# Kernel optimization log

Hardware: AMD Instinct MI355X
Metric: run time of the kernel (lower is better)

## Reference

```python
import jax, jax.numpy as jnp
import numpy as np

NUM_ITER = 4
MIN_DISP = 1.0 / 100.0  # 1/max_depth
MAX_DISP = 1.0 / 0.1    # 1/min_depth


def _diag_embed(v):
    return v[..., :, None] * jnp.eye(v.shape[-1], dtype=v.dtype)


def _v2m(r):  # r: [B,3,1] -> antisymmetric [B,3,3]
    a1, a2, a3 = r[:, 0, 0], r[:, 1, 0], r[:, 2, 0]
    z = jnp.zeros_like(a1)
    return jnp.stack([z, -a3, a2, a3, z, -a1, -a2, a1, z], axis=-1).reshape(-1, 3, 3)


def _se3_pose(se3):  # se3: [B,6,1] -> [B,3,4]
    B = se3.shape[0]
    t, w = se3[:, 0:3], se3[:, 3:6]
    Nr = jnp.maximum(jnp.sqrt(jnp.sum(w * w, axis=1, keepdims=True)), 1e-12)  # [B,1,1]
    r = w / Nr
    I = jnp.eye(3, dtype=se3.dtype)[None]
    rx = _v2m(r)
    c, s = jnp.cos(Nr), jnp.sin(Nr)
    R = c * I + (1.0 - c) * jnp.matmul(r, jnp.transpose(r, (0, 2, 1))) + s * rx
    J = I + (Nr - s) / Nr * jnp.matmul(rx, rx) + (1.0 - c) / Nr * rx
    T = jnp.matmul(J, t)
    return jnp.concatenate([R, T], axis=2)


def _homogeneous(p34):
    B = p34.shape[0]
    ext = jnp.broadcast_to(jnp.array([[[0.0, 0.0, 0.0, 1.0]]], dtype=p34.dtype), (B, 1, 4))
    return jnp.concatenate([p34, ext], axis=1)


def _project_2d3d(points, depth, K_inv):  # [B,2,N],[B,1,N] -> [B,3,N]
    ones = jnp.ones_like(points[:, :1])
    xy3d = jnp.concatenate([points, ones], axis=1)
    return jnp.matmul(K_inv, xy3d) * depth


def _project_3d2d(p3d, K):
    q = jnp.matmul(K, p3d)
    return q[:, 0:2] / jnp.maximum(q[:, 2:3], 0.01)


def _reproject_error(p1, p2, disp, pose, K, K_inv):
    depth = 1.0 / jnp.maximum(disp, 0.01)
    p3d = _project_2d3d(p1, depth, K_inv)
    p3d_hat = jnp.matmul(pose[:, :3, :3], p3d) + pose[:, :3, 3:]
    return p2 - _project_3d2d(p3d_hat, K)


def _mean_on_mask(data, mask):  # reduce over last (point) dim, keepdims
    return jnp.sum(data * mask, axis=2, keepdims=True) / jnp.sum(mask, axis=2, keepdims=True)


def _jacobi_pose(p3d, K):  # -> [B,2,6,N]
    B, _, N = p3d.shape
    fx, fy = K[:, 0:1, 0:1], K[:, 1:2, 1:2]
    X, Y = p3d[:, 0:1], p3d[:, 1:2]
    Z = jnp.maximum(p3d[:, 2:3], 1e-12)
    iZ = 1.0 / Z
    iZ2 = iZ * iZ
    z = jnp.zeros_like(X)
    rows = [fx * iZ, z, -fx * X * iZ2, -fx * X * Y * iZ2, fx + fx * X * X * iZ2, -fx * Y * iZ,
            z, fy * iZ, -fy * Y * iZ2, -fy - fy * Y * Y * iZ2, fy * X * Y * iZ2, fy * X * iZ]
    return -jnp.concatenate(rows, axis=1).reshape(B, 2, 6, N)


def _jacobi_disp(p3d, pose, disps):  # -> [B,2,1,N]
    B, _, N = p3d.shape
    fx, fy = K0 = pose  # placeholder avoided below
    raise NotImplementedError


def _jacobi_disp_impl(p3d, pose, K, disps):  # -> [B,2,1,N]
    B, _, N = p3d.shape
    fx, fy = K[:, 0:1, 0:1], K[:, 1:2, 1:2]
    X, Y = p3d[:, 0:1], p3d[:, 1:2]
    Z = jnp.maximum(p3d[:, 2:3], 1e-12)
    iZ = 1.0 / Z
    iZ2 = iZ * iZ
    z = jnp.zeros_like(X)
    J1 = jnp.concatenate([fx * iZ, z, -fx * X * iZ2, z, fy * iZ, -fy * Y * iZ2], axis=1)
    J1 = jnp.transpose(J1.reshape(B, 2, 3, N), (0, 3, 1, 2))  # [B,N,2,3]
    T = pose[:, :3, 3:]  # [B,3,1]
    DD = -1.0 / disps    # [B,1,N]
    J2 = jnp.concatenate([DD * (X - T[:, 0:1]), (Y - T[:, 1:2]) * DD, (Z - T[:, 2:3]) * DD], axis=1)
    J2 = jnp.transpose(J2.reshape(B, 3, 1, N), (0, 3, 1, 2))  # [B,N,3,1]
    J = -jnp.matmul(J1, J2)                                   # [B,N,2,1]
    return jnp.transpose(J, (0, 2, 3, 1))                     # [B,2,1,N]


def _huber_w(err, mask, b=9.0):  # diag values of the [B,N,2,2] weight -> [B,N,2]
    B, _, N = err.shape
    en = jnp.sqrt(jnp.sum(err * err, axis=1, keepdims=True))          # [B,1,N]
    w = jnp.minimum(b / jnp.maximum(en, 1e-12), 1.0)
    w = jnp.sqrt(w) * mask                                            # [B,1,N]
    w = jnp.broadcast_to(jnp.transpose(w, (0, 2, 1)), (B, N, 2))
    return jax.lax.stop_gradient(w)


def _marginalization(Bm, E, C, V, W, L):
    Bsz, N = E.shape[0], E.shape[1]
    Bm = Bm + _diag_embed(jnp.diagonal(Bm, axis1=-2, axis2=-1)) * L   # L:[B,1,1]
    C = C + C * L.reshape(Bsz, 1, 1, 1)                               # C diag is itself (1x1)
    C_inv = 1.0 / jnp.maximum(C, 1.0)
    Bm = Bm + jnp.eye(6, dtype=Bm.dtype)
    Ev = E[..., 0]                 # [B,N,6]
    cinv = C_inv[:, :, 0, 0]       # [B,N]
    Wv = W[:, :, 0, 0]             # [B,N]
    Hsc = jnp.einsum('bn,bni,bnj->bij', cinv, Ev, Ev) / N
    bsc = (jnp.einsum('bn,bni,bn->bi', cinv, Ev, Wv) / N)[..., None]  # [B,6,1]
    invL = 1.0 / (1.0 + L)
    left = Bm - Hsc * invL
    right = V - bsc * invL
    s = 1.0 / jnp.sqrt(jnp.diagonal(left, axis1=-2, axis2=-1) + 10.0)  # [B,6]
    D = _diag_embed(s)
    H = D @ left @ D
    delta_pose = D @ jnp.linalg.solve(H, D @ right)                   # [B,6,1]
    p3d_sc = jnp.einsum('bni,bi->bn', Ev, delta_pose[:, :, 0]) * invL[:, 0, 0][:, None]
    delta_points = cinv * (Wv - p3d_sc)                               # [B,N]
    return delta_pose, delta_points


def _lm_step(pts_coord, pts_disp, pose, K, K_inv, mask, L):
    B, _, N = pts_coord.shape
    pts_depth = 1.0 / pts_disp
    p3d = _project_2d3d(pts_coord[:, 0:2], pts_depth, K_inv)
    p3d_hat = jnp.matmul(pose[:, :3, :3], p3d) + pose[:, :3, 3:]
    p2d_hat = _project_3d2d(p3d_hat, K)
    errors = pts_coord[:, 2:4] - p2d_hat                     # [B,2,N]
    J_pose = _jacobi_pose(p3d_hat, K)                        # [B,2,6,N]
    J_disp = _jacobi_disp_impl(p3d_hat, pose, K, pts_disp)   # [B,2,1,N]
    w = _huber_w(errors, mask)                               # [B,N,2]
    w2 = w * w
    Jp_T = jnp.transpose(J_pose, (0, 3, 2, 1))               # [B,N,6,2]
    Jd_T = jnp.transpose(J_disp, (0, 3, 2, 1))               # [B,N,1,2]
    Jp = jnp.transpose(J_pose, (0, 3, 1, 2))                 # [B,N,2,6]
    Jd = jnp.transpose(J_disp, (0, 3, 1, 2))                 # [B,N,2,1]
    Bm = jnp.einsum('bnik,bnkj->bij', Jp_T * w2[:, :, None, :], Jp) / N
    E = jnp.matmul(Jp_T * w2[:, :, None, :], Jd)             # [B,N,6,1]
    C = jnp.matmul(Jd_T * w2[:, :, None, :], Jd)             # [B,N,1,1]
    e = jnp.transpose(errors, (0, 2, 1))[..., None]          # [B,N,2,1]
    g_pose = -jnp.einsum('bnik,bnkj->bij', Jp_T * w[:, :, None, :], e) / N  # [B,6,1]
    g_disp = -jnp.matmul(Jd_T * w[:, :, None, :], e)         # [B,N,1,1]
    delta_pose, delta_points = _marginalization(Bm, E, C, g_pose, g_disp, L)
    return delta_pose, delta_points[:, None, :]              # [B,6,1], [B,1,N]


def reference(pts_coord, pts_disp, pose, K, K_inv, mask, L):
    for _ in range(NUM_ITER):
        dp, dd = _lm_step(pts_coord, pts_disp, pose, K, K_inv, mask, L)
        disp_new = jnp.clip(pts_disp + dd, MIN_DISP, MAX_DISP)
        pose_new = jnp.matmul(_homogeneous(_se3_pose(dp)), pose)
        e1 = _reproject_error(pts_coord[:, 0:2], pts_coord[:, 2:4], disp_new, pose_new, K, K_inv)
        e2 = _reproject_error(pts_coord[:, 0:2], pts_coord[:, 2:4], pts_disp, pose, K, K_inv)
        r1 = _mean_on_mask(jnp.linalg.norm(e1, axis=1, keepdims=True), mask)
        r2 = _mean_on_mask(jnp.linalg.norm(e2, axis=1, keepdims=True), mask)
        M = jax.lax.stop_gradient((r1 < r2).astype(pose.dtype))  # [B,1,1]
        pts_disp = jnp.where(M == 1, disp_new, pts_disp)
        pose = jnp.where(M == 1, pose_new, pose)
        L = jnp.clip(jnp.where(M == 1, L * 0.5, L * 5.0), 0.01, 1e6)
    return pose, pts_disp


def setup_inputs() -> dict:
    B, N = 8, 131072
    W, H = 640, 480
    key = jax.random.key(0)
    k = jax.random.split(key, 4)
    p1 = jax.random.uniform(k[0], (B, 2, N), dtype=jnp.float32) * jnp.array([W, H], jnp.float32).reshape(1, 2, 1)
    p2 = p1 + jax.random.normal(k[1], (B, 2, N), dtype=jnp.float32) * 2.0
    pts_coord = jnp.concatenate([p1, p2], axis=1)                      # [B,4,N]
    pts_disp = jax.random.uniform(k[2], (B, 1, N), dtype=jnp.float32, minval=0.05, maxval=2.0)
    pose = jnp.tile(jnp.eye(4, dtype=jnp.float32)[None], (B, 1, 1))
    pose = pose.at[:, :3, 3].set(jax.random.normal(k[3], (B, 3), dtype=jnp.float32) * 0.05)
    K = jnp.tile(jnp.array([[320.0, 0.0, 320.0], [0.0, 320.0, 240.0], [0.0, 0.0, 1.0]], jnp.float32)[None], (B, 1, 1))
    K_inv = jnp.linalg.inv(K)
    mask = jnp.ones((B, 1, N), jnp.float32)
    L = jnp.ones((B, 1, 1), jnp.float32) * 0.01
    return {'pts_coord': pts_coord, 'pts_disp': pts_disp, 'pose': pose, 'K': K, 'K_inv': K_inv, 'mask': mask, 'L': L}
```

## Files before the change

kernel.cpp:

```cpp
#include <hip/hip_runtime.h>
#include <math.h>


constexpr int TPB  = 256;
constexpr int BLKA = 64;
constexpr int NRED = 54;

__device__ __forceinline__ float wave_red(float v) {
#pragma unroll
  for (int m = 32; m; m >>= 1) v += __shfl_xor(v, m, 64);
  return v;
}

__device__ __forceinline__ float reproj_norm(
    float x1, float y1, float x2, float y2, float d,
    const float* P, const float* Kc, const float* Ki) {
  float depth = 1.0f / fmaxf(d, 0.01f);
  float pxx = (Ki[0]*x1 + Ki[1]*y1 + Ki[2]) * depth;
  float pyy = (Ki[3]*x1 + Ki[4]*y1 + Ki[5]) * depth;
  float pzz = (Ki[6]*x1 + Ki[7]*y1 + Ki[8]) * depth;
  float X = P[0]*pxx + P[1]*pyy + P[2]*pzz + P[3];
  float Y = P[4]*pxx + P[5]*pyy + P[6]*pzz + P[7];
  float Z = P[8]*pxx + P[9]*pyy + P[10]*pzz + P[11];
  float q0 = Kc[0]*X + Kc[1]*Y + Kc[2]*Z;
  float q1 = Kc[3]*X + Kc[4]*Y + Kc[5]*Z;
  float q2 = Kc[6]*X + Kc[7]*Y + Kc[8]*Z;
  float iZc = 1.0f / fmaxf(q2, 0.01f);
  float ex = x2 - q0*iZc, ey = y2 - q1*iZc;
  return sqrtf(ex*ex + ey*ey);
}

__global__ __launch_bounds__(TPB) void kpassA(
    const float* __restrict__ pts, const float* __restrict__ disp_src,
    const float* __restrict__ prop, const float* __restrict__ mask,
    const float* __restrict__ Kin, const float* __restrict__ Kiin,
    float* __restrict__ disp_cur, const float* __restrict__ pose_cur,
    const float* __restrict__ Lc, const float* __restrict__ flags,
    float* __restrict__ partA, int N) {
  const int b = blockIdx.y;
  float Kc[9], Ki[9], P[12];
#pragma unroll
  for (int i = 0; i < 9; i++) { Kc[i] = Kin[b*9+i]; Ki[i] = Kiin[b*9+i]; }
#pragma unroll
  for (int i = 0; i < 12; i++) P[i] = pose_cur[b*16+i];
  const float Lval = Lc[b];
  const float onepL = 1.0f + Lval;
  const float fsel = flags[b];
  const float fx = Kc[0], fy = Kc[4];

  float acc[NRED];
#pragma unroll
  for (int k = 0; k < NRED; k++) acc[k] = 0.0f;

  const size_t bN = (size_t)b * N;
  const float* px1 = pts + (size_t)b*4*N;
  const float* py1 = px1 + N;
  const float* px2 = px1 + 2*(size_t)N;
  const float* py2 = px1 + 3*(size_t)N;

  for (int n = blockIdx.x*TPB + threadIdx.x; n < N; n += gridDim.x*TPB) {
    float x1 = px1[n], y1 = py1[n], x2 = px2[n], y2 = py2[n];
    float d = disp_src[bN+n];
    if (fsel != 0.0f) d = prop[bN+n];
    disp_cur[bN+n] = d;
    float m = mask[bN+n];

    float depth = 1.0f / d;
    float pxx = (Ki[0]*x1 + Ki[1]*y1 + Ki[2]) * depth;
    float pyy = (Ki[3]*x1 + Ki[4]*y1 + Ki[5]) * depth;
    float pzz = (Ki[6]*x1 + Ki[7]*y1 + Ki[8]) * depth;
    float X = P[0]*pxx + P[1]*pyy + P[2]*pzz + P[3];
    float Y = P[4]*pxx + P[5]*pyy + P[6]*pzz + P[7];
    float Z = P[8]*pxx + P[9]*pyy + P[10]*pzz + P[11];
    float q0 = Kc[0]*X + Kc[1]*Y + Kc[2]*Z;
    float q1 = Kc[3]*X + Kc[4]*Y + Kc[5]*Z;
    float q2 = Kc[6]*X + Kc[7]*Y + Kc[8]*Z;
    float iZc = 1.0f / fmaxf(q2, 0.01f);
    float ex = x2 - q0*iZc;
    float ey = y2 - q1*iZc;
    float iZ = 1.0f / fmaxf(Z, 1e-12f);
    float iZ2 = iZ*iZ;

    float jp0[6], jp1[6];
    jp0[0] = -(fx*iZ);  jp0[1] = 0.0f;       jp0[2] = fx*X*iZ2;
    jp0[3] = fx*X*Y*iZ2; jp0[4] = -(fx + fx*X*X*iZ2); jp0[5] = fx*Y*iZ;
    jp1[0] = 0.0f;      jp1[1] = -(fy*iZ);   jp1[2] = fy*Y*iZ2;
    jp1[3] = fy + fy*Y*Y*iZ2; jp1[4] = -(fy*X*Y*iZ2); jp1[5] = -(fy*X*iZ);

    float DD = -depth;
    float dx = X - P[3], dy = Y - P[7], dz = Z - P[11];
    float jd0 = -((fx*iZ)*(DD*dx) - (fx*X*iZ2)*(DD*dz));
    float jd1 = -((fy*iZ)*(DD*dy) - (fy*Y*iZ2)*(DD*dz));

    float en = sqrtf(ex*ex + ey*ey);
    float wmin = fminf(9.0f / fmaxf(en, 1e-12f), 1.0f);
    float w  = sqrtf(wmin) * m;
    float w2 = w * w;

    float E[6];
#pragma unroll
    for (int k = 0; k < 6; k++) E[k] = w2*(jp0[k]*jd0 + jp1[k]*jd1);
    float C = w2*(jd0*jd0 + jd1*jd1);
    float cinv = 1.0f / fmaxf(C*onepL, 1.0f);
    float Wv = -w*(jd0*ex + jd1*ey);

    int idx = 0;
#pragma unroll
    for (int k = 0; k < 6; k++)
#pragma unroll
      for (int l = k; l < 6; l++) { acc[idx] += w2*(jp0[k]*jp0[l] + jp1[k]*jp1[l]); idx++; }
#pragma unroll
    for (int k = 0; k < 6; k++) acc[21+k] -= w*(jp0[k]*ex + jp1[k]*ey);
    idx = 27;
#pragma unroll
    for (int k = 0; k < 6; k++)
#pragma unroll
      for (int l = k; l < 6; l++) { acc[idx] += (cinv*E[k])*E[l]; idx++; }
#pragma unroll
    for (int k = 0; k < 6; k++) acc[48+k] += cinv*E[k]*Wv;
  }

  __shared__ float lds[TPB/64][NRED];
  const int lane = threadIdx.x & 63, wvi = threadIdx.x >> 6;
#pragma unroll
  for (int k = 0; k < NRED; k++) {
    float v = wave_red(acc[k]);
    if (lane == 0) lds[wvi][k] = v;
  }
  __syncthreads();
  if (threadIdx.x < NRED) {
    float s = 0.0f;
#pragma unroll
    for (int wq = 0; wq < TPB/64; wq++) s += lds[wq][threadIdx.x];
    partA[((size_t)b*gridDim.x + blockIdx.x)*NRED + threadIdx.x] = s;
  }
}

__global__ __launch_bounds__(64) void ksolve(
    const float* __restrict__ partA, int nblk,
    const float* __restrict__ Lc, const float* __restrict__ pose_cur,
    float* __restrict__ pose_new, float* __restrict__ dpose, int N) {
  const int b = blockIdx.x;
  __shared__ float S[NRED];
  const int t = threadIdx.x;
  if (t < NRED) {
    float s = 0.0f;
    for (int j = 0; j < nblk; j++) s += partA[((size_t)b*nblk + j)*NRED + t];
    S[t] = s;
  }
  __syncthreads();
  if (t != 0) return;

  const float invN = 1.0f / (float)N;
  float Bm[6][6], Hs[6][6], g[6], bs[6];
  {
    int idx = 0;
    for (int k = 0; k < 6; k++)
      for (int l = k; l < 6; l++) { float v = S[idx++]*invN; Bm[k][l] = v; Bm[l][k] = v; }
    for (int k = 0; k < 6; k++) g[k] = S[21+k]*invN;
    idx = 27;
    for (int k = 0; k < 6; k++)
      for (int l = k; l < 6; l++) { float v = S[idx++]*invN; Hs[k][l] = v; Hs[l][k] = v; }
    for (int k = 0; k < 6; k++) bs[k] = S[48+k]*invN;
  }
  const float L = Lc[b];
  const float invL = 1.0f / (1.0f + L);
  float left[6][6], right[6];
  for (int k = 0; k < 6; k++) {
    for (int l = 0; l < 6; l++) {
      float v = Bm[k][l] - Hs[k][l]*invL;
      if (k == l) v += Bm[k][k]*L + 1.0f;
      left[k][l] = v;
    }
    right[k] = g[k] - bs[k]*invL;
  }
  float sv[6];
  for (int k = 0; k < 6; k++) sv[k] = 1.0f / sqrtf(left[k][k] + 10.0f);
  float H[6][7];
  for (int k = 0; k < 6; k++) {
    for (int l = 0; l < 6; l++) H[k][l] = sv[k]*left[k][l]*sv[l];
    H[k][6] = sv[k]*right[k];
  }
  for (int c = 0; c < 6; c++) {
    int piv = c; float mx = fabsf(H[c][c]);
    for (int r = c+1; r < 6; r++) { float a = fabsf(H[r][c]); if (a > mx) { mx = a; piv = r; } }
    if (piv != c)
      for (int cc2 = c; cc2 < 7; cc2++) { float tmp = H[c][cc2]; H[c][cc2] = H[piv][cc2]; H[piv][cc2] = tmp; }
    float ip = 1.0f / H[c][c];
    for (int r = c+1; r < 6; r++) {
      float f = H[r][c]*ip;
      for (int cc2 = c; cc2 < 7; cc2++) H[r][cc2] -= f*H[c][cc2];
    }
  }
  float x[6];
  for (int c = 5; c >= 0; c--) {
    float v = H[c][6];
    for (int cc2 = c+1; cc2 < 6; cc2++) v -= H[c][cc2]*x[cc2];
    x[c] = v / H[c][c];
  }
  float dp[6];
  for (int k = 0; k < 6; k++) { dp[k] = sv[k]*x[k]; dpose[b*6+k] = dp[k]; }

  float tx = dp[0], ty = dp[1], tz = dp[2];
  float wx = dp[3], wy = dp[4], wz = dp[5];
  float Nr = fmaxf(sqrtf(wx*wx + wy*wy + wz*wz), 1e-12f);
  float rx = wx/Nr, ry = wy/Nr, rz = wz/Nr;
  float c_ = cosf(Nr), sn = sinf(Nr);
  float omc = 1.0f - c_;
  float SK[3][3] = {{0.0f,-rz,ry},{rz,0.0f,-rx},{-ry,rx,0.0f}};
  float SK2[3][3];
  for (int i = 0; i < 3; i++)
    for (int j = 0; j < 3; j++) {
      float s2 = 0.0f;
      for (int k = 0; k < 3; k++) s2 += SK[i][k]*SK[k][j];
      SK2[i][j] = s2;
    }
  float rr[3] = {rx, ry, rz};
  float a = (Nr - sn)/Nr, bcoef = omc/Nr;
  float R3[3][3], Jm[3][3];
  for (int i = 0; i < 3; i++)
    for (int j = 0; j < 3; j++) {
      float eye = (i == j) ? 1.0f : 0.0f;
      R3[i][j] = c_*eye + omc*rr[i]*rr[j] + sn*SK[i][j];
      Jm[i][j] = eye + a*SK2[i][j] + bcoef*SK[i][j];
    }
  float T3[3];
  for (int i = 0; i < 3; i++) T3[i] = Jm[i][0]*tx + Jm[i][1]*ty + Jm[i][2]*tz;
  float Pc[16];
  for (int i = 0; i < 16; i++) Pc[i] = pose_cur[b*16+i];
  float Pn[16];
  for (int i = 0; i < 3; i++)
    for (int j = 0; j < 4; j++)
      Pn[i*4+j] = R3[i][0]*Pc[j] + R3[i][1]*Pc[4+j] + R3[i][2]*Pc[8+j] + T3[i]*Pc[12+j];
  for (int j = 0; j < 4; j++) Pn[12+j] = Pc[12+j];
  for (int i = 0; i < 16; i++) pose_new[b*16+i] = Pn[i];
}

__global__ __launch_bounds__(TPB) void kpassB(
    const float* __restrict__ pts, const float* __restrict__ disp_cur,
    const float* __restrict__ mask,
    const float* __restrict__ Kin, const float* __restrict__ Kiin,
    const float* __restrict__ pose_cur, const float* __restrict__ pose_new,
    const float* __restrict__ Lc, const float* __restrict__ dpose,
    float* __restrict__ prop, float* __restrict__ partB, int N) {
  const int b = blockIdx.y;
  float Kc[9], Ki[9], P[12], Pn[12], dp[6];
#pragma unroll
  for (int i = 0; i < 9; i++) { Kc[i] = Kin[b*9+i]; Ki[i] = Kiin[b*9+i]; }
#pragma unroll
  for (int i = 0; i < 12; i++) { P[i] = pose_cur[b*16+i]; Pn[i] = pose_new[b*16+i]; }
#pragma unroll
  for (int i = 0; i < 6; i++) dp[i] = dpose[b*6+i];
  const float Lval = Lc[b];
  const float onepL = 1.0f + Lval;
  const float invL = 1.0f / onepL;
  const float fx = Kc[0], fy = Kc[4];

  float r1a = 0.0f, r2a = 0.0f, msa = 0.0f;
  const size_t bN = (size_t)b * N;
  const float* px1 = pts + (size_t)b*4*N;
  const float* py1 = px1 + N;
  const float* px2 = px1 + 2*(size_t)N;
  const float* py2 = px1 + 3*(size_t)N;

  for (int n = blockIdx.x*TPB + threadIdx.x; n < N; n += gridDim.x*TPB) {
    float x1 = px1[n], y1 = py1[n], x2 = px2[n], y2 = py2[n];
    float d = disp_cur[bN+n];
    float m = mask[bN+n];

    float depth = 1.0f / d;
    float pxx = (Ki[0]*x1 + Ki[1]*y1 + Ki[2]) * depth;
    float pyy = (Ki[3]*x1 + Ki[4]*y1 + Ki[5]) * depth;
    float pzz = (Ki[6]*x1 + Ki[7]*y1 + Ki[8]) * depth;
    float X = P[0]*pxx + P[1]*pyy + P[2]*pzz + P[3];
    float Y = P[4]*pxx + P[5]*pyy + P[6]*pzz + P[7];
    float Z = P[8]*pxx + P[9]*pyy + P[10]*pzz + P[11];
    float q0 = Kc[0]*X + Kc[1]*Y + Kc[2]*Z;
    float q1 = Kc[3]*X + Kc[4]*Y + Kc[5]*Z;
    float q2 = Kc[6]*X + Kc[7]*Y + Kc[8]*Z;
    float iZc = 1.0f / fmaxf(q2, 0.01f);
    float ex = x2 - q0*iZc;
    float ey = y2 - q1*iZc;
    float iZ = 1.0f / fmaxf(Z, 1e-12f);
    float iZ2 = iZ*iZ;

    float jp0[6], jp1[6];
    jp0[0] = -(fx*iZ);  jp0[1] = 0.0f;       jp0[2] = fx*X*iZ2;
    jp0[3] = fx*X*Y*iZ2; jp0[4] = -(fx + fx*X*X*iZ2); jp0[5] = fx*Y*iZ;
    jp1[0] = 0.0f;      jp1[1] = -(fy*iZ);   jp1[2] = fy*Y*iZ2;
    jp1[3] = fy + fy*Y*Y*iZ2; jp1[4] = -(fy*X*Y*iZ2); jp1[5] = -(fy*X*iZ);

    float DD = -depth;
    float dx = X - P[3], dy = Y - P[7], dz = Z - P[11];
    float jd0 = -((fx*iZ)*(DD*dx) - (fx*X*iZ2)*(DD*dz));
    float jd1 = -((fy*iZ)*(DD*dy) - (fy*Y*iZ2)*(DD*dz));

    float en = sqrtf(ex*ex + ey*ey);
    float wmin = fminf(9.0f / fmaxf(en, 1e-12f), 1.0f);
    float w  = sqrtf(wmin) * m;
    float w2 = w * w;

    float dotE = 0.0f;
#pragma unroll
    for (int k = 0; k < 6; k++) {
      float Ek = w2*(jp0[k]*jd0 + jp1[k]*jd1);
      dotE += Ek * dp[k];
    }
    float C = w2*(jd0*jd0 + jd1*jd1);
    float cinv = 1.0f / fmaxf(C*onepL, 1.0f);
    float Wv = -w*(jd0*ex + jd1*ey);

    float dnew = d + cinv*(Wv - dotE*invL);
    dnew = fminf(fmaxf(dnew, 0.01f), 10.0f);
    prop[bN+n] = dnew;

    float n1 = reproj_norm(x1, y1, x2, y2, dnew, Pn, Kc, Ki);
    float n2 = reproj_norm(x1, y1, x2, y2, d,    P,  Kc, Ki);
    r1a += n1*m; r2a += n2*m; msa += m;
  }

  __shared__ float lds[TPB/64][3];
  const int lane = threadIdx.x & 63, wvi = threadIdx.x >> 6;
  float v0 = wave_red(r1a), v1 = wave_red(r2a), v2 = wave_red(msa);
  if (lane == 0) { lds[wvi][0] = v0; lds[wvi][1] = v1; lds[wvi][2] = v2; }
  __syncthreads();
  if (threadIdx.x < 3) {
    float s = 0.0f;
#pragma unroll
    for (int wq = 0; wq < TPB/64; wq++) s += lds[wq][threadIdx.x];
    partB[((size_t)b*gridDim.x + blockIdx.x)*3 + threadIdx.x] = s;
  }
}

__global__ __launch_bounds__(256) void kupdate(
    int iter, const float* __restrict__ partB, int nblk,
    const float* __restrict__ pose_in, const float* __restrict__ L_in,
    float* __restrict__ pose_cur, const float* __restrict__ pose_new,
    float* __restrict__ Lc, float* __restrict__ flags, int B) {
  const int t = threadIdx.x;
  if (iter == 0) {
    if (t < B*16) pose_cur[t] = pose_in[t];
    if (t < B) { Lc[t] = L_in[t]; flags[t] = 0.0f; }
    return;
  }
  __shared__ float sM[16];
  if (t < B) {
    float r1 = 0.0f, r2 = 0.0f, ms = 0.0f;
    for (int j = 0; j < nblk; j++) {
      const float* p = partB + ((size_t)t*nblk + j)*3;
      r1 += p[0]; r2 += p[1]; ms += p[2];
    }
    float M = ((r1/ms) < (r2/ms)) ? 1.0f : 0.0f;
    sM[t] = M;
    flags[t] = M;
    float L = Lc[t];
    L = (M != 0.0f) ? L*0.5f : L*5.0f;
    Lc[t] = fminf(fmaxf(L, 0.01f), 1000000.0f);
  }
  __syncthreads();
  if (t < B*16) {
    int b = t >> 4;
    if (sM[b] != 0.0f) pose_cur[t] = pose_new[t];
  }
}

__global__ __launch_bounds__(TPB) void kout(
    const float* __restrict__ pose_cur, const float* __restrict__ flags,
    const float* __restrict__ prop, float* __restrict__ dout, int N, int B) {
  const int b = blockIdx.y;
  if (blockIdx.x == 0 && threadIdx.x < 16)
    dout[b*16 + threadIdx.x] = pose_cur[b*16 + threadIdx.x];
  if (flags[b] == 0.0f) return;
  float* dd = dout + B*16;
  const size_t bN = (size_t)b * N;
  for (int n = blockIdx.x*TPB + threadIdx.x; n < N; n += gridDim.x*TPB)
    dd[bN+n] = prop[bN+n];
}

extern "C" void kernel_launch(void* const* d_in, const int* in_sizes, int n_in,
                              void* d_out, int out_size, void* d_ws, size_t ws_size,
                              hipStream_t stream) {
  const float* pts   = (const float*)d_in[0];
  const float* disp0 = (const float*)d_in[1];
  const float* pose0 = (const float*)d_in[2];
  const float* Kin   = (const float*)d_in[3];
  const float* Kiin  = (const float*)d_in[4];
  const float* mask  = (const float*)d_in[5];
  const float* L0    = (const float*)d_in[6];

  const int B = in_sizes[6];
  const int N = in_sizes[1] / B;
  const size_t BN = (size_t)B * N;

  float* out      = (float*)d_out;
  float* disp_cur = out + B*16;

  float* ws       = (float*)d_ws;
  float* prop     = ws;
  float* partA    = prop + BN;
  float* partB    = partA + (size_t)B*BLKA*NRED;
  float* pose_cur = partB + (size_t)B*BLKA*3;
  float* pose_new = pose_cur + (size_t)B*16;
  float* Lc       = pose_new + (size_t)B*16;
  float* dpose    = Lc + B;
  float* flags    = dpose + (size_t)B*6;

  dim3 gridBig(BLKA, B), blk(TPB);
  for (int it = 0; it < 4; ++it) {
    kupdate<<<1, 256, 0, stream>>>(it, partB, BLKA, pose0, L0,
                                   pose_cur, pose_new, Lc, flags, B);
    kpassA<<<gridBig, blk, 0, stream>>>(pts, (it == 0) ? disp0 : disp_cur, prop,
                                        mask, Kin, Kiin, disp_cur, pose_cur,
                                        Lc, flags, partA, N);
    ksolve<<<dim3(B), dim3(64), 0, stream>>>(partA, BLKA, Lc, pose_cur,
                                             pose_new, dpose, N);
    kpassB<<<gridBig, blk, 0, stream>>>(pts, disp_cur, mask, Kin, Kiin,
                                        pose_cur, pose_new, Lc, dpose,
                                        prop, partB, N);
  }
  kupdate<<<1, 256, 0, stream>>>(4, partB, BLKA, pose0, L0,
                                 pose_cur, pose_new, Lc, flags, B);
  kout<<<gridBig, blk, 0, stream>>>(pose_cur, flags, prop, out, N, B);
}
```

Baseline: 349.5 us.

## Fold solve and update kernels into the streaming passes via redundant per-block compute

Drops the tiny kupdate and ksolve launches. Each block of the main passes now recomputes the accept decision, the damping update and the 6x6 LM solve redundantly, and block 0 persists the shared state. Pose and L are double-buffered across iterations so no block reads state that another block in the same kernel is writing. This cuts the launch count per iteration from 4 to 2, removing launch gaps, at the cost of serial single-thread solve work and extra partial-sum reads at the start of every block.

```diff
diff --git a/kernel.cpp b/kernel.cpp
--- a/kernel.cpp
+++ b/kernel.cpp
@@ -30,22 +30,61 @@
   return sqrtf(ex*ex + ey*ey);
 }
 
-__global__ __launch_bounds__(TPB) void kpassA(
+__device__ __forceinline__ float accept_M(const float* __restrict__ partB,
+                                          int b) {
+  float r1 = 0.0f, r2 = 0.0f, ms = 0.0f;
+  for (int j = 0; j < BLKA; j++) {
+    const float* p = partB + ((size_t)b*BLKA + j)*3;
+    r1 += p[0]; r2 += p[1]; ms += p[2];
+  }
+  return ((r1/ms) < (r2/ms)) ? 1.0f : 0.0f;
+}
+
+__global__ __launch_bounds__(TPB) void kA(
+    int it,
     const float* __restrict__ pts, const float* __restrict__ disp_src,
     const float* __restrict__ prop, const float* __restrict__ mask,
     const float* __restrict__ Kin, const float* __restrict__ Kiin,
-    float* __restrict__ disp_cur, const float* __restrict__ pose_cur,
-    const float* __restrict__ Lc, const float* __restrict__ flags,
+    float* __restrict__ disp_cur,
+    const float* __restrict__ pose0, const float* __restrict__ L0,
+    const float* __restrict__ partB, const float* __restrict__ pose_new_ws,
+    float* __restrict__ pose_slot_w, const float* __restrict__ pose_slot_r,
+    float* __restrict__ L_slot_w, const float* __restrict__ L_slot_r,
     float* __restrict__ partA, int N) {
   const int b = blockIdx.y;
+
+  __shared__ float sP[16];
+  __shared__ float sMeta[2];
+  if (threadIdx.x == 0) {
+    float P[16], Lv, fs;
+    if (it == 0) {
+      for (int i = 0; i < 16; i++) P[i] = pose0[b*16+i];
+      Lv = L0[b]; fs = 0.0f;
+    } else {
+      float M = accept_M(partB, b);
+      fs = M;
+      float Lp = L_slot_r[b];
+      float Ln = (M != 0.0f) ? Lp*0.5f : Lp*5.0f;
+      Lv = fminf(fmaxf(Ln, 0.01f), 1000000.0f);
+      for (int i = 0; i < 16; i++)
+        P[i] = (M != 0.0f) ? pose_new_ws[b*16+i] : pose_slot_r[b*16+i];
+    }
+    for (int i = 0; i < 16; i++) sP[i] = P[i];
+    sMeta[0] = fs; sMeta[1] = Lv;
+    if (blockIdx.x == 0) {
+      for (int i = 0; i < 16; i++) pose_slot_w[b*16+i] = P[i];
+      L_slot_w[b] = Lv;
+    }
+  }
+  __syncthreads();
+
   float Kc[9], Ki[9], P[12];
 #pragma unroll
   for (int i = 0; i < 9; i++) { Kc[i] = Kin[b*9+i]; Ki[i] = Kiin[b*9+i]; }
 #pragma unroll
-  for (int i = 0; i < 12; i++) P[i] = pose_cur[b*16+i];
-  const float Lval = Lc[b];
-  const float onepL = 1.0f + Lval;
-  const float fsel = flags[b];
+  for (int i = 0; i < 12; i++) P[i] = sP[i];
+  const float onepL = 1.0f + sMeta[1];
+  const float fsel = sMeta[0];
   const float fx = Kc[0], fy = Kc[4];
 
   float acc[NRED];
@@ -136,123 +175,123 @@
   }
 }
 
-__global__ __launch_bounds__(64) void ksolve(
-    const float* __restrict__ partA, int nblk,
-    const float* __restrict__ Lc, const float* __restrict__ pose_cur,
-    float* __restrict__ pose_new, float* __restrict__ dpose, int N) {
-  const int b = blockIdx.x;
-  __shared__ float S[NRED];
-  const int t = threadIdx.x;
-  if (t < NRED) {
-    float s = 0.0f;
-    for (int j = 0; j < nblk; j++) s += partA[((size_t)b*nblk + j)*NRED + t];
-    S[t] = s;
-  }
-  __syncthreads();
-  if (t != 0) return;
-
-  const float invN = 1.0f / (float)N;
-  float Bm[6][6], Hs[6][6], g[6], bs[6];
-  {
-    int idx = 0;
-    for (int k = 0; k < 6; k++)
-      for (int l = k; l < 6; l++) { float v = S[idx++]*invN; Bm[k][l] = v; Bm[l][k] = v; }
-    for (int k = 0; k < 6; k++) g[k] = S[21+k]*invN;
-    idx = 27;
-    for (int k = 0; k < 6; k++)
-      for (int l = k; l < 6; l++) { float v = S[idx++]*invN; Hs[k][l] = v; Hs[l][k] = v; }
-    for (int k = 0; k < 6; k++) bs[k] = S[48+k]*invN;
-  }
-  const float L = Lc[b];
-  const float invL = 1.0f / (1.0f + L);
-  float left[6][6], right[6];
-  for (int k = 0; k < 6; k++) {
-    for (int l = 0; l < 6; l++) {
-      float v = Bm[k][l] - Hs[k][l]*invL;
-      if (k == l) v += Bm[k][k]*L + 1.0f;
-      left[k][l] = v;
-    }
-    right[k] = g[k] - bs[k]*invL;
-  }
-  float sv[6];
-  for (int k = 0; k < 6; k++) sv[k] = 1.0f / sqrtf(left[k][k] + 10.0f);
-  float H[6][7];
-  for (int k = 0; k < 6; k++) {
-    for (int l = 0; l < 6; l++) H[k][l] = sv[k]*left[k][l]*sv[l];
-    H[k][6] = sv[k]*right[k];
-  }
-  for (int c = 0; c < 6; c++) {
-    int piv = c; float mx = fabsf(H[c][c]);
-    for (int r = c+1; r < 6; r++) { float a = fabsf(H[r][c]); if (a > mx) { mx = a; piv = r; } }
-    if (piv != c)
-      for (int cc2 = c; cc2 < 7; cc2++) { float tmp = H[c][cc2]; H[c][cc2] = H[piv][cc2]; H[piv][cc2] = tmp; }
-    float ip = 1.0f / H[c][c];
-    for (int r = c+1; r < 6; r++) {
-      float f = H[r][c]*ip;
-      for (int cc2 = c; cc2 < 7; cc2++) H[r][cc2] -= f*H[c][cc2];
-    }
-  }
-  float x[6];
-  for (int c = 5; c >= 0; c--) {
-    float v = H[c][6];
-    for (int cc2 = c+1; cc2 < 6; cc2++) v -= H[c][cc2]*x[cc2];
-    x[c] = v / H[c][c];
-  }
-  float dp[6];
-  for (int k = 0; k < 6; k++) { dp[k] = sv[k]*x[k]; dpose[b*6+k] = dp[k]; }
-
-  float tx = dp[0], ty = dp[1], tz = dp[2];
-  float wx = dp[3], wy = dp[4], wz = dp[5];
-  float Nr = fmaxf(sqrtf(wx*wx + wy*wy + wz*wz), 1e-12f);
-  float rx = wx/Nr, ry = wy/Nr, rz = wz/Nr;
-  float c_ = cosf(Nr), sn = sinf(Nr);
-  float omc = 1.0f - c_;
-  float SK[3][3] = {{0.0f,-rz,ry},{rz,0.0f,-rx},{-ry,rx,0.0f}};
-  float SK2[3][3];
-  for (int i = 0; i < 3; i++)
-    for (int j = 0; j < 3; j++) {
-      float s2 = 0.0f;
-      for (int k = 0; k < 3; k++) s2 += SK[i][k]*SK[k][j];
-      SK2[i][j] = s2;
-    }
-  float rr[3] = {rx, ry, rz};
-  float a = (Nr - sn)/Nr, bcoef = omc/Nr;
-  float R3[3][3], Jm[3][3];
-  for (int i = 0; i < 3; i++)
-    for (int j = 0; j < 3; j++) {
-      float eye = (i == j) ? 1.0f : 0.0f;
-      R3[i][j] = c_*eye + omc*rr[i]*rr[j] + sn*SK[i][j];
-      Jm[i][j] = eye + a*SK2[i][j] + bcoef*SK[i][j];
-    }
-  float T3[3];
-  for (int i = 0; i < 3; i++) T3[i] = Jm[i][0]*tx + Jm[i][1]*ty + Jm[i][2]*tz;
-  float Pc[16];
-  for (int i = 0; i < 16; i++) Pc[i] = pose_cur[b*16+i];
-  float Pn[16];
-  for (int i = 0; i < 3; i++)
-    for (int j = 0; j < 4; j++)
-      Pn[i*4+j] = R3[i][0]*Pc[j] + R3[i][1]*Pc[4+j] + R3[i][2]*Pc[8+j] + T3[i]*Pc[12+j];
-  for (int j = 0; j < 4; j++) Pn[12+j] = Pc[12+j];
-  for (int i = 0; i < 16; i++) pose_new[b*16+i] = Pn[i];
-}
-
-__global__ __launch_bounds__(TPB) void kpassB(
+__global__ __launch_bounds__(TPB) void kB(
     const float* __restrict__ pts, const float* __restrict__ disp_cur,
     const float* __restrict__ mask,
     const float* __restrict__ Kin, const float* __restrict__ Kiin,
-    const float* __restrict__ pose_cur, const float* __restrict__ pose_new,
-    const float* __restrict__ Lc, const float* __restrict__ dpose,
+    const float* __restrict__ pose_slot, const float* __restrict__ L_slot,
+    const float* __restrict__ partA,
+    float* __restrict__ pose_new_ws,
     float* __restrict__ prop, float* __restrict__ partB, int N) {
   const int b = blockIdx.y;
+  const float L = L_slot[b];
+
+  __shared__ float S[NRED];
+  __shared__ float sPn[16];
+  __shared__ float sdp[6];
+  if (threadIdx.x < NRED) {
+    float s = 0.0f;
+    for (int j = 0; j < BLKA; j++)
+      s += partA[((size_t)b*BLKA + j)*NRED + threadIdx.x];
+    S[threadIdx.x] = s;
+  }
+  __syncthreads();
+  if (threadIdx.x == 0) {
+    const float invN = 1.0f / (float)N;
+    float Bm[6][6], Hs[6][6], g[6], bs[6];
+    {
+      int idx = 0;
+      for (int k = 0; k < 6; k++)
+        for (int l = k; l < 6; l++) { float v = S[idx++]*invN; Bm[k][l] = v; Bm[l][k] = v; }
+      for (int k = 0; k < 6; k++) g[k] = S[21+k]*invN;
+      idx = 27;
+      for (int k = 0; k < 6; k++)
+        for (int l = k; l < 6; l++) { float v = S[idx++]*invN; Hs[k][l] = v; Hs[l][k] = v; }
+      for (int k = 0; k < 6; k++) bs[k] = S[48+k]*invN;
+    }
+    const float invL = 1.0f / (1.0f + L);
+    float left[6][6], right[6];
+    for (int k = 0; k < 6; k++) {
+      for (int l = 0; l < 6; l++) {
+        float v = Bm[k][l] - Hs[k][l]*invL;
+        if (k == l) v += Bm[k][k]*L + 1.0f;
+        left[k][l] = v;
+      }
+      right[k] = g[k] - bs[k]*invL;
+    }
+    float sv[6];
+    for (int k = 0; k < 6; k++) sv[k] = 1.0f / sqrtf(left[k][k] + 10.0f);
+    float H[6][7];
+    for (int k = 0; k < 6; k++) {
+      for (int l = 0; l < 6; l++) H[k][l] = sv[k]*left[k][l]*sv[l];
+      H[k][6] = sv[k]*right[k];
+    }
+    for (int c = 0; c < 6; c++) {
+      int piv = c; float mx = fabsf(H[c][c]);
+      for (int r = c+1; r < 6; r++) { float a = fabsf(H[r][c]); if (a > mx) { mx = a; piv = r; } }
+      if (piv != c)
+        for (int cc2 = c; cc2 < 7; cc2++) { float tmp = H[c][cc2]; H[c][cc2] = H[piv][cc2]; H[piv][cc2] = tmp; }
+      float ip = 1.0f / H[c][c];
+      for (int r = c+1; r < 6; r++) {
+        float f = H[r][c]*ip;
+        for (int cc2 = c; cc2 < 7; cc2++) H[r][cc2] -= f*H[c][cc2];
+      }
+    }
+    float x[6];
+    for (int c = 5; c >= 0; c--) {
+      float v = H[c][6];
+      for (int cc2 = c+1; cc2 < 6; cc2++) v -= H[c][cc2]*x[cc2];
+      x[c] = v / H[c][c];
+    }
+    float dp[6];
+    for (int k = 0; k < 6; k++) { dp[k] = sv[k]*x[k]; sdp[k] = dp[k]; }
+
+    float tx = dp[0], ty = dp[1], tz = dp[2];
+    float wx = dp[3], wy = dp[4], wz = dp[5];
+    float Nr = fmaxf(sqrtf(wx*wx + wy*wy + wz*wz), 1e-12f);
+    float rx = wx/Nr, ry = wy/Nr, rz = wz/Nr;
+    float c_ = cosf(Nr), sn = sinf(Nr);
+    float omc = 1.0f - c_;
+    float SK[3][3] = {{0.0f,-rz,ry},{rz,0.0f,-rx},{-ry,rx,0.0f}};
+    float SK2[3][3];
+    for (int i = 0; i < 3; i++)
+      for (int j = 0; j < 3; j++) {
+        float s2 = 0.0f;
+        for (int k = 0; k < 3; k++) s2 += SK[i][k]*SK[k][j];
+        SK2[i][j] = s2;
+      }
+    float rr[3] = {rx, ry, rz};
+    float a = (Nr - sn)/Nr, bcoef = omc/Nr;
+    float R3[3][3], Jm[3][3];
+    for (int i = 0; i < 3; i++)
+      for (int j = 0; j < 3; j++) {
+        float eye = (i == j) ? 1.0f : 0.0f;
+        R3[i][j] = c_*eye + omc*rr[i]*rr[j] + sn*SK[i][j];
+        Jm[i][j] = eye + a*SK2[i][j] + bcoef*SK[i][j];
+      }
+    float T3[3];
+    for (int i = 0; i < 3; i++) T3[i] = Jm[i][0]*tx + Jm[i][1]*ty + Jm[i][2]*tz;
+    float Pc[16];
+    for (int i = 0; i < 16; i++) Pc[i] = pose_slot[b*16+i];
+    float Pn[16];
+    for (int i = 0; i < 3; i++)
+      for (int j = 0; j < 4; j++)
+        Pn[i*4+j] = R3[i][0]*Pc[j] + R3[i][1]*Pc[4+j] + R3[i][2]*Pc[8+j] + T3[i]*Pc[12+j];
+    for (int j = 0; j < 4; j++) Pn[12+j] = Pc[12+j];
+    for (int i = 0; i < 16; i++) sPn[i] = Pn[i];
+    if (blockIdx.x == 0)
+      for (int i = 0; i < 16; i++) pose_new_ws[b*16+i] = Pn[i];
+  }
+  __syncthreads();
+
   float Kc[9], Ki[9], P[12], Pn[12], dp[6];
 #pragma unroll
   for (int i = 0; i < 9; i++) { Kc[i] = Kin[b*9+i]; Ki[i] = Kiin[b*9+i]; }
 #pragma unroll
-  for (int i = 0; i < 12; i++) { P[i] = pose_cur[b*16+i]; Pn[i] = pose_new[b*16+i]; }
-#pragma unroll
-  for (int i = 0; i < 6; i++) dp[i] = dpose[b*6+i];
-  const float Lval = Lc[b];
-  const float onepL = 1.0f + Lval;
+  for (int i = 0; i < 12; i++) { P[i] = pose_slot[b*16+i]; Pn[i] = sPn[i]; }
+#pragma unroll
+  for (int i = 0; i < 6; i++) dp[i] = sdp[i];
+  const float onepL = 1.0f + L;
   const float invL = 1.0f / onepL;
   const float fx = Kc[0], fy = Kc[4];
 
@@ -332,45 +371,21 @@
   }
 }
 
-__global__ __launch_bounds__(256) void kupdate(
-    int iter, const float* __restrict__ partB, int nblk,
-    const float* __restrict__ pose_in, const float* __restrict__ L_in,
-    float* __restrict__ pose_cur, const float* __restrict__ pose_new,
-    float* __restrict__ Lc, float* __restrict__ flags, int B) {
-  const int t = threadIdx.x;
-  if (iter == 0) {
-    if (t < B*16) pose_cur[t] = pose_in[t];
-    if (t < B) { Lc[t] = L_in[t]; flags[t] = 0.0f; }
-    return;
-  }
-  __shared__ float sM[16];
-  if (t < B) {
-    float r1 = 0.0f, r2 = 0.0f, ms = 0.0f;
-    for (int j = 0; j < nblk; j++) {
-      const float* p = partB + ((size_t)t*nblk + j)*3;
-      r1 += p[0]; r2 += p[1]; ms += p[2];
-    }
-    float M = ((r1/ms) < (r2/ms)) ? 1.0f : 0.0f;
-    sM[t] = M;
-    flags[t] = M;
-    float L = Lc[t];
-    L = (M != 0.0f) ? L*0.5f : L*5.0f;
-    Lc[t] = fminf(fmaxf(L, 0.01f), 1000000.0f);
-  }
-  __syncthreads();
-  if (t < B*16) {
-    int b = t >> 4;
-    if (sM[b] != 0.0f) pose_cur[t] = pose_new[t];
-  }
-}
-
-__global__ __launch_bounds__(TPB) void kout(
-    const float* __restrict__ pose_cur, const float* __restrict__ flags,
+__global__ __launch_bounds__(TPB) void kF(
+    const float* __restrict__ partB,
+    const float* __restrict__ pose_slot, const float* __restrict__ pose_new_ws,
     const float* __restrict__ prop, float* __restrict__ dout, int N, int B) {
   const int b = blockIdx.y;
-  if (blockIdx.x == 0 && threadIdx.x < 16)
-    dout[b*16 + threadIdx.x] = pose_cur[b*16 + threadIdx.x];
-  if (flags[b] == 0.0f) return;
+  __shared__ float sM[1];
+  if (threadIdx.x == 0) sM[0] = accept_M(partB, b);
+  __syncthreads();
+  const float M = sM[0];
+
+  if (blockIdx.x == 0 && threadIdx.x < 16) {
+    float v = (M != 0.0f) ? pose_new_ws[b*16+threadIdx.x] : pose_slot[b*16+threadIdx.x];
+    dout[b*16 + threadIdx.x] = v;
+  }
+  if (M == 0.0f) return;
   float* dd = dout + B*16;
   const size_t bN = (size_t)b * N;
   for (int n = blockIdx.x*TPB + threadIdx.x; n < N; n += gridDim.x*TPB)
@@ -395,30 +410,29 @@
   float* out      = (float*)d_out;
   float* disp_cur = out + B*16;
 
-  float* ws       = (float*)d_ws;
-  float* prop     = ws;
-  float* partA    = prop + BN;
-  float* partB    = partA + (size_t)B*BLKA*NRED;
-  float* pose_cur = partB + (size_t)B*BLKA*3;
-  float* pose_new = pose_cur + (size_t)B*16;
-  float* Lc       = pose_new + (size_t)B*16;
-  float* dpose    = Lc + B;
-  float* flags    = dpose + (size_t)B*6;
+  float* ws        = (float*)d_ws;
+  float* prop      = ws;
+  float* partA     = prop + BN;
+  float* partB     = partA + (size_t)B*BLKA*NRED;
+  float* pose_slots= partB + (size_t)B*BLKA*3;
+  float* pose_new  = pose_slots + (size_t)2*B*16;
+  float* L_slots   = pose_new + (size_t)B*16;
 
   dim3 gridBig(BLKA, B), blk(TPB);
   for (int it = 0; it < 4; ++it) {
-    kupdate<<<1, 256, 0, stream>>>(it, partB, BLKA, pose0, L0,
-                                   pose_cur, pose_new, Lc, flags, B);
-    kpassA<<<gridBig, blk, 0, stream>>>(pts, (it == 0) ? disp0 : disp_cur, prop,
-                                        mask, Kin, Kiin, disp_cur, pose_cur,
-                                        Lc, flags, partA, N);
-    ksolve<<<dim3(B), dim3(64), 0, stream>>>(partA, BLKA, Lc, pose_cur,
-                                             pose_new, dpose, N);
-    kpassB<<<gridBig, blk, 0, stream>>>(pts, disp_cur, mask, Kin, Kiin,
-                                        pose_cur, pose_new, Lc, dpose,
-                                        prop, partB, N);
-  }
-  kupdate<<<1, 256, 0, stream>>>(4, partB, BLKA, pose0, L0,
-                                 pose_cur, pose_new, Lc, flags, B);
-  kout<<<gridBig, blk, 0, stream>>>(pose_cur, flags, prop, out, N, B);
-}
+    float* ps_w = pose_slots + (size_t)(it & 1) * B * 16;
+    const float* ps_r = pose_slots + (size_t)((it + 1) & 1) * B * 16;
+    float* Ls_w = L_slots + (size_t)(it & 1) * B;
+    const float* Ls_r = L_slots + (size_t)((it + 1) & 1) * B;
+
+    kA<<<gridBig, blk, 0, stream>>>(it, pts, (it == 0) ? disp0 : disp_cur, prop,
+                                    mask, Kin, Kiin, disp_cur, pose0, L0,
+                                    partB, pose_new, ps_w, ps_r, Ls_w, Ls_r,
+                                    partA, N);
+    kB<<<gridBig, blk, 0, stream>>>(pts, disp_cur, mask, Kin, Kiin,
+                                    ps_w, Ls_w, partA, pose_new,
+                                    prop, partB, N);
+  }
+  kF<<<gridBig, blk, 0, stream>>>(partB, pose_slots + (size_t)1*B*16, pose_new,
+                                  prop, out, N, B);
+}
```

Measured after the change: 285.4 us. 1.22x faster.
